# Kernel optimization log

Measured on AMD Instinct MI355X. Metric: run time of the kernel, lower is better.

## Reference

```python
import jax, jax.numpy as jnp
import numpy as np
from jax.ops import segment_sum, segment_max

N_NODES = 100000
N_EDGES = 1600000
F_DIM = 64
N_GRAPHS = 64
K_HOPS = 3
EPS = 1e-5


def setup_inputs() -> dict:
    key = jax.random.key(0)
    ks = jax.random.split(key, 8)
    x = jax.random.normal(ks[0], (N_NODES, F_DIM), dtype=jnp.float32)
    edge_index = jax.random.randint(ks[1], (2, N_EDGES), 0, N_NODES, dtype=jnp.int32)
    batch = jnp.sort(jax.random.randint(ks[2], (N_NODES,), 0, N_GRAPHS, dtype=jnp.int32))
    edge_weight = jax.random.uniform(ks[3], (N_EDGES,), dtype=jnp.float32)
    # TAGConv params: K+1 hop-wise linear weights (no per-lin bias) + one output bias
    W = jax.random.normal(ks[4], (K_HOPS + 1, F_DIM, F_DIM), dtype=jnp.float32) * 0.05
    b = jnp.zeros((F_DIM,), dtype=jnp.float32)
    # GraphNorm params
    gn_weight = jnp.ones((F_DIM,), dtype=jnp.float32)
    gn_bias = jnp.zeros((F_DIM,), dtype=jnp.float32)
    gn_mean_scale = jnp.ones((F_DIM,), dtype=jnp.float32)
    return {"x": x, "edge_index": edge_index, "batch": batch, "edge_weight": edge_weight,
            "W": W, "b": b, "gn_weight": gn_weight, "gn_bias": gn_bias,
            "gn_mean_scale": gn_mean_scale}


def reference(x, edge_index, batch, edge_weight, W, b, gn_weight, gn_bias, gn_mean_scale):
    src, dst = edge_index[0], edge_index[1]

    # --- TAGConv: gcn_norm without self-loops ---
    deg = segment_sum(edge_weight, dst, num_segments=N_NODES)            # [N]
    dis = jnp.where(deg > 0, jax.lax.rsqrt(deg), 0.0)                    # deg^{-1/2}, inf -> 0
    norm = dis[src] * edge_weight * dis[dst]                             # [E]

    # out = sum_k (A_norm^k x) W_k + b
    out = x @ W[0]
    h = x
    for k in range(1, K_HOPS + 1):
        h = segment_sum(norm[:, None] * h[src], dst, num_segments=N_NODES)  # [N, F]
        out = out + h @ W[k]
    out = out + b

    # --- GraphNorm: per-graph mean/var with learnable mean_scale ---
    cnt = segment_sum(jnp.ones((N_NODES,), out.dtype), batch, num_segments=N_GRAPHS)
    cnt = jnp.maximum(cnt, 1.0)[:, None]                                  # [G, 1]
    mean = segment_sum(out, batch, num_segments=N_GRAPHS) / cnt          # [G, F]
    centered = out - mean[batch] * gn_mean_scale                         # [N, F]
    var = segment_sum(centered * centered, batch, num_segments=N_GRAPHS) / cnt
    hn = gn_weight * centered / jnp.sqrt(var + EPS)[batch] + gn_bias

    # --- residual + ReLU (add_residue=True) ---
    h_emb = jax.nn.relu(hn + x)                                          # [N, F]

    # --- global mean + max pooling ---
    mean_pool = segment_sum(h_emb, batch, num_segments=N_GRAPHS) / cnt   # [G, F]
    max_pool = segment_max(h_emb, batch, num_segments=N_GRAPHS)          # [G, F]
    flat = jnp.concatenate([mean_pool, max_pool], axis=-1)               # [G, 2F]

    return (h_emb, flat)
```

## Files before the change

### kernel.cpp

```cpp
#include <hip/hip_runtime.h>
#include <hip/hip_bf16.h>

#define NN 100000
#define NE 1600000
#define NG 64
#define FD 64
#define EPSV 1e-5f

typedef __hip_bfloat16 bf16;
typedef __attribute__((ext_vector_type(8))) short bf16x8;
typedef __attribute__((ext_vector_type(4))) float f32x4;

__device__ __forceinline__ float ldb(bf16 v) { return __bfloat162float(v); }
__device__ __forceinline__ bf16 f2b(float v) { return __float2bfloat16(v); }
__device__ __forceinline__ float b2f_bits(short s) {
    return __uint_as_float(((unsigned)(unsigned short)s) << 16);
}

#define NB1 391
#define CB 625
#define EPB 2560
#define CCN (NB1 * CB)
#define SCB2 ((CCN + 2047) / 2048)

__device__ __forceinline__ int xcd_chunk(int bid, int nwg) {
    int q = nwg >> 3, r = nwg & 7;
    int xcd = bid & 7, j = bid >> 3;
    return (xcd < r ? xcd * (q + 1) : r * (q + 1) + (xcd - r) * q) + j;
}

constexpr size_t ALGN(size_t x) { return (x + 255) & ~(size_t)255; }
constexpr size_t OFF_GSUM = 0;
constexpr size_t OFF_GSSQ = OFF_GSUM + ALGN((size_t)NG * FD * 4);
constexpr size_t OFF_GCNT = OFF_GSSQ + ALGN((size_t)NG * FD * 4);
constexpr size_t OFF_PSUM = OFF_GCNT + ALGN((size_t)NG * 4);
constexpr size_t OFF_PMAX = OFF_PSUM + ALGN((size_t)NG * FD * 4);
constexpr size_t ZERO_BYTES = OFF_PMAX + ALGN((size_t)NG * FD * 4);
constexpr size_t OFF_CNT  = ZERO_BYTES;
constexpr size_t OFF_DIS  = OFF_CNT  + ALGN((size_t)NN * 4);
constexpr size_t OFF_ROWP = OFF_DIS  + ALGN((size_t)NN * 4);
constexpr size_t OFF_BSUM = OFF_ROWP + ALGN((size_t)NN * 4);
constexpr size_t OFF_WT   = OFF_BSUM + ALGN(256 * 4);
constexpr size_t OFF_CSR  = OFF_WT   + ALGN(16384 * 2);
constexpr size_t OFF_H    = OFF_CSR  + ALGN((size_t)NE * 8);
constexpr size_t OFF_OUT  = OFF_H    + ALGN((size_t)NN * 256 * 2);
constexpr size_t OFF_CSRT = OFF_OUT;
constexpr size_t OFF_CC   = OFF_CSRT + ALGN((size_t)NE * 8);
static_assert(OFF_CC + (size_t)CCN * 4 - OFF_OUT <= (size_t)NN * FD * 4, "alias overflow");

#define XCB 25000
__global__ __launch_bounds__(256) void coarse_fused_kernel(const int* __restrict__ dst,
                                                           int* __restrict__ cc,
                                                           const float* __restrict__ x,
                                                           bf16* __restrict__ H,
                                                           const float* __restrict__ W,
                                                           bf16* __restrict__ Wt) {
    int b = blockIdx.x;
    if (b < CB) {
        __shared__ int hist[NB1];
        for (int i = threadIdx.x; i < NB1; i += 256) hist[i] = 0;
        __syncthreads();
        int e0 = b * EPB + threadIdx.x;
        #pragma unroll
        for (int i = 0; i < EPB / 256; i++)
            atomicAdd(&hist[dst[e0 + i * 256] >> 8], 1);
        __syncthreads();
        for (int i = threadIdx.x; i < NB1; i += 256)
            cc[(size_t)i * CB + b] = hist[i];
    } else if (b < CB + XCB) {
        int i = (b - CB) * 256 + threadIdx.x;
        if (i >= NN * 64) return;
        int node = i >> 6, f = i & 63;
        H[(size_t)node * 256 + f] = f2b(x[(size_t)node * 64 + f]);
    } else {
        int i = (b - CB - XCB) * 256 + threadIdx.x;
        int n = i & 63, kk = i >> 6;
        Wt[n * 256 + kk] = f2b(W[kk * 64 + n]);
    }
}

#define SCAN_BLK 256
#define SCAN_ITEMS 8
__global__ __launch_bounds__(SCAN_BLK) void scan_blocks(int* __restrict__ data,
                                                        int* __restrict__ bsum, int n) {
    __shared__ int lds[SCAN_BLK];
    int t = threadIdx.x, b = blockIdx.x;
    int base = b * SCAN_BLK * SCAN_ITEMS + t * SCAN_ITEMS;
    int v[SCAN_ITEMS];
    int s = 0;
    #pragma unroll
    for (int i = 0; i < SCAN_ITEMS; i++) {
        int idx = base + i;
        v[i] = (idx < n) ? data[idx] : 0;
        s += v[i];
    }
    lds[t] = s;
    __syncthreads();
    for (int off = 1; off < SCAN_BLK; off <<= 1) {
        int x = (t >= off) ? lds[t - off] : 0;
        __syncthreads();
        lds[t] += x;
        __syncthreads();
    }
    int excl = lds[t] - s;
    if (t == SCAN_BLK - 1) bsum[b] = lds[t];
    int run = excl;
    #pragma unroll
    for (int i = 0; i < SCAN_ITEMS; i++) {
        int idx = base + i;
        if (idx < n) data[idx] = run;
        run += v[i];
    }
}

__global__ __launch_bounds__(256) void bsum_scan(int* __restrict__ bsum, int nb) {
    __shared__ int lds[256];
    int t = threadIdx.x;
    int v = (t < nb) ? bsum[t] : 0;
    lds[t] = v;
    __syncthreads();
    for (int off = 1; off < 256; off <<= 1) {
        int x = (t >= off) ? lds[t - off] : 0;
        __syncthreads();
        lds[t] += x;
        __syncthreads();
    }
    if (t < nb) bsum[t] = lds[t] - v;
}

__global__ __launch_bounds__(256) void scan_add2(int* __restrict__ data,
                                                 const int* __restrict__ bpref, int n) {
    int i = blockIdx.x * 256 + threadIdx.x;
    if (i >= n) return;
    data[i] += bpref[i >> 11];
}

__global__ __launch_bounds__(256) void scatter2_kernel(const int* __restrict__ src,
                                                       const int* __restrict__ dst,
                                                       const float* __restrict__ ew,
                                                       const int* __restrict__ cc,
                                                       int2* __restrict__ csrt) {
    __shared__ int sc[512];
    __shared__ int gdel[NB1];
    __shared__ int2 stage[EPB];
    __shared__ int sdel[EPB];
    int t = threadIdx.x;
    int L = xcd_chunk(blockIdx.x, CB);

    sc[t] = 0; sc[t + 256] = 0;
    __syncthreads();

    int br[EPB / 256], px[EPB / 256], pw[EPB / 256];
    #pragma unroll
    for (int i = 0; i < EPB / 256; i++) {
        int e = L * EPB + i * 256 + t;
        int d = dst[e];
        int bk = d >> 8;
        int rk = atomicAdd(&sc[bk], 1);
        br[i] = bk | (rk << 9);
        px[i] = src[e] | ((d & 255) << 17);
        pw[i] = __float_as_int(ew[e]);
    }
    __syncthreads();

    for (int off = 1; off < 512; off <<= 1) {
        int a0 = (t >= off) ? sc[t - off] : 0;
        int a1 = sc[t + 256 - off];
        __syncthreads();
        sc[t] += a0; sc[t + 256] += a1;
        __syncthreads();
    }

    for (int i = t; i < NB1; i += 256)
        gdel[i] = cc[(size_t)i * CB + L] - ((i > 0) ? sc[i - 1] : 0);
    __syncthreads();

    #pragma unroll
    for (int i = 0; i < EPB / 256; i++) {
        int bk = br[i] & 511;
        int rk = br[i] >> 9;
        int slot = ((bk > 0) ? sc[bk - 1] : 0) + rk;
        stage[slot] = make_int2(px[i], pw[i]);
        sdel[slot] = gdel[bk];
    }
    __syncthreads();

    for (int j = t; j < EPB; j += 256)
        csrt[(size_t)(sdel[j] + j)] = stage[j];
}

__global__ __launch_bounds__(256) void fine_kernel(const int* __restrict__ cc,
                                                   const int2* __restrict__ csrt,
                                                   int2* __restrict__ csr,
                                                   int* __restrict__ rowp,
                                                   int* __restrict__ cnts,
                                                   float* __restrict__ dis) {
    __shared__ int hist[256];
    __shared__ float degw[256];
    __shared__ int pref[256];
    __shared__ int fcur[256];
    int b = blockIdx.x;
    int t = threadIdx.x;
    int base = cc[(size_t)b * CB];
    int end = (b == NB1 - 1) ? NE : cc[(size_t)(b + 1) * CB];
    int cnt = end - base;
    hist[t] = 0; degw[t] = 0.f;
    __syncthreads();
    for (int j = t; j < cnt; j += 256) {
        int2 e = csrt[base + j];
        int f = e.x >> 17;
        atomicAdd(&hist[f], 1);
        atomicAdd(&degw[f], __int_as_float(e.y));
    }
    __syncthreads();
    int hv = hist[t];
    pref[t] = hv;
    __syncthreads();
    for (int off = 1; off < 256; off <<= 1) {
        int x = (t >= off) ? pref[t - off] : 0;
        __syncthreads();
        pref[t] += x;
        __syncthreads();
    }
    int ex = pref[t] - hv;
    fcur[t] = ex;
    int node = b * 256 + t;
    if (node < NN) {
        rowp[node] = base + ex;
        cnts[node] = hv;
        float s = degw[t];
        dis[node] = (s > 0.f) ? rsqrtf(s) : 0.f;
    }
    __syncthreads();
    for (int j = t; j < cnt; j += 256) {
        int2 e = csrt[base + j];
        int f = e.x >> 17;
        int pos = atomicAdd(&fcur[f], 1);
        csr[base + pos] = make_int2(e.x & 0x1FFFF, e.y);
    }
}

template <bool FIRST>
__global__ __launch_bounds__(256) void hop_kernel(const bf16* __restrict__ hin,
                                                  bf16* __restrict__ hout,
                                                  const int* __restrict__ rowp,
                                                  const int* __restrict__ cnts,
                                                  int2* __restrict__ csr,
                                                  const float* __restrict__ dis) {
    int row = blockIdx.x * 4 + (threadIdx.x >> 6);
    if (row >= NN) return;
    row = __builtin_amdgcn_readfirstlane(row);
    int lane = threadIdx.x & 63;
    int sub = lane >> 3;
    int fl = lane & 7;
    int start = rowp[row];
    int cnt = cnts[row];
    float dr = dis[row];
    int2* cp = csr + start;

    float a[8] = {0, 0, 0, 0, 0, 0, 0, 0};

    if (cnt <= 24) {
        int2 e0 = (sub < cnt) ? cp[sub] : make_int2(0, 0);
        int2 e1 = (8 + sub < cnt) ? cp[8 + sub] : make_int2(0, 0);
        int2 e2 = (16 + sub < cnt) ? cp[16 + sub] : make_int2(0, 0);
        bf16x8 v0 = *(const bf16x8*)(hin + (size_t)e0.x * 256 + fl * 8);
        bf16x8 v1 = *(const bf16x8*)(hin + (size_t)e1.x * 256 + fl * 8);
        bf16x8 v2 = *(const bf16x8*)(hin + (size_t)e2.x * 256 + fl * 8);
        float w0 = __int_as_float(e0.y);
        float w1 = __int_as_float(e1.y);
        float w2 = __int_as_float(e2.y);
        if (FIRST) {
            w0 *= dis[e0.x]; w1 *= dis[e1.x]; w2 *= dis[e2.x];
            if (fl == 0) {
                if (sub < cnt)      cp[sub].y      = __float_as_int(w0);
                if (8 + sub < cnt)  cp[8 + sub].y  = __float_as_int(w1);
                if (16 + sub < cnt) cp[16 + sub].y = __float_as_int(w2);
            }
        }
        #pragma unroll
        for (int i = 0; i < 8; i++)
            a[i] = w0 * b2f_bits(v0[i]) + w1 * b2f_bits(v1[i]) + w2 * b2f_bits(v2[i]);
    } else {
        float b[8] = {0, 0, 0, 0, 0, 0, 0, 0};
        int j = 0;
        for (; j + 16 <= cnt; j += 16) {
            int2 e0 = cp[j + sub];
            int2 e1 = cp[j + 8 + sub];
            bf16x8 v0 = *(const bf16x8*)(hin + (size_t)e0.x * 256 + fl * 8);
            bf16x8 v1 = *(const bf16x8*)(hin + (size_t)e1.x * 256 + fl * 8);
            float w0 = __int_as_float(e0.y);
            float w1 = __int_as_float(e1.y);
            if (FIRST) {
                w0 *= dis[e0.x]; w1 *= dis[e1.x];
                if (fl == 0) {
                    cp[j + sub].y     = __float_as_int(w0);
                    cp[j + 8 + sub].y = __float_as_int(w1);
                }
            }
            #pragma unroll
            for (int i = 0; i < 8; i++) a[i] += w0 * b2f_bits(v0[i]);
            #pragma unroll
            for (int i = 0; i < 8; i++) b[i] += w1 * b2f_bits(v1[i]);
        }
        for (; j < cnt; j += 8) {
            int jj = j + sub;
            int2 e = (jj < cnt) ? cp[jj] : make_int2(0, 0);
            bf16x8 v = *(const bf16x8*)(hin + (size_t)e.x * 256 + fl * 8);
            float w = __int_as_float(e.y);
            if (FIRST) {
                w *= dis[e.x];
                if (fl == 0 && jj < cnt) cp[jj].y = __float_as_int(w);
            }
            #pragma unroll
            for (int i = 0; i < 8; i++) a[i] += w * b2f_bits(v[i]);
        }
        #pragma unroll
        for (int i = 0; i < 8; i++) a[i] += b[i];
    }

    #pragma unroll
    for (int i = 0; i < 8; i++) a[i] += __shfl_xor(a[i], 8);
    #pragma unroll
    for (int i = 0; i < 8; i++) a[i] += __shfl_xor(a[i], 16);
    #pragma unroll
    for (int i = 0; i < 8; i++) a[i] += __shfl_xor(a[i], 32);

    if (sub == 0) {
        bf16x8 ov;
        #pragma unroll
        for (int i = 0; i < 8; i++) {
            bf16 t = f2b(a[i] * dr);
            ov[i] = *(short*)&t;
        }
        *(bf16x8*)(hout + (size_t)row * 256 + fl * 8) = ov;
    }
}

__global__ __launch_bounds__(256) void gemm_kernel(const bf16* __restrict__ H,
                                                   const bf16* __restrict__ Wt,
                                                   const float* __restrict__ bias,
                                                   float* __restrict__ outb) {
    int row0 = blockIdx.x * 16;
    int wave = threadIdx.x >> 6;
    int lane = threadIdx.x & 63;
    int m = lane & 15, q = lane >> 4;
    int c0 = wave * 16;

    bf16x8 A[8];
    const bf16* arow = H + (size_t)(row0 + m) * 256 + q * 8;
    #pragma unroll
    for (int ks = 0; ks < 8; ks++)
        A[ks] = *(const bf16x8*)(arow + ks * 32);

    const bf16* brow = Wt + (size_t)(c0 + m) * 256 + q * 8;
    f32x4 acc = {0.f, 0.f, 0.f, 0.f};
    #pragma unroll
    for (int ks = 0; ks < 8; ks++) {
        bf16x8 B = *(const bf16x8*)(brow + ks * 32);
        acc = __builtin_amdgcn_mfma_f32_16x16x32_bf16(A[ks], B, acc, 0, 0, 0);
    }

    float bv = bias[c0 + m];
    #pragma unroll
    for (int r = 0; r < 4; r++)
        outb[(size_t)(row0 + q * 4 + r) * 64 + c0 + m] = acc[r] + bv;
}

#define CH 32
#define STAT_WAVES ((NN + CH - 1) / CH)
#define STAT_BLOCKS ((STAT_WAVES * 64 + 255) / 256)

__global__ __launch_bounds__(256) void stats_kernel(const float* __restrict__ outb,
                                                    const int* __restrict__ batch,
                                                    float* __restrict__ gsum,
                                                    float* __restrict__ gssq,
                                                    float* __restrict__ gcnt) {
    int wid = (blockIdx.x * 256 + threadIdx.x) >> 6;
    int lane = threadIdx.x & 63;
    int n0 = wid * CH;
    if (n0 >= NN) return;
    int n1 = min(n0 + CH, NN);
    int g0 = batch[n0];
    if (n1 == n0 + CH && batch[n1 - 1] == g0) {
        float s = 0.f, s2 = 0.f;
        #pragma unroll
        for (int i = 0; i < CH; i++) {
            float v = outb[(size_t)(n0 + i) * 64 + lane];
            s += v; s2 += v * v;
        }
        atomicAdd(&gsum[g0 * 64 + lane], s);
        atomicAdd(&gssq[g0 * 64 + lane], s2);
        if (lane == 0) atomicAdd(&gcnt[g0], (float)CH);
    } else {
        int cur = g0; float s = 0.f, s2 = 0.f; int cl = 0;
        for (int i = n0; i < n1; i++) {
            int g = batch[i];
            if (g != cur) {
                atomicAdd(&gsum[cur * 64 + lane], s);
                atomicAdd(&gssq[cur * 64 + lane], s2);
                if (lane == 0) atomicAdd(&gcnt[cur], (float)cl);
                s = 0.f; s2 = 0.f; cl = 0; cur = g;
            }
            float v = outb[(size_t)i * 64 + lane];
            s += v; s2 += v * v; cl++;
        }
        atomicAdd(&gsum[cur * 64 + lane], s);
        atomicAdd(&gssq[cur * 64 + lane], s2);
        if (lane == 0) atomicAdd(&gcnt[cur], (float)cl);
    }
}

__device__ __forceinline__ void graph_mr(const float* gsum, const float* gssq,
                                         const float* gcnt, int g, int lane, float ms,
                                         float& mm, float& r) {
    float c = fmaxf(gcnt[g], 1.f);
    float mean = gsum[g * 64 + lane] / c;
    float msq = gssq[g * 64 + lane] / c;
    mm = mean * ms;
    float var = fmaxf(msq - 2.f * mm * mean + mm * mm, 0.f);
    r = rsqrtf(var + EPSV);
}

__global__ __launch_bounds__(256) void final_kernel(const float* __restrict__ outb,
                                                    const int* __restrict__ batch,
                                                    const float* __restrict__ xg,
                                                    const float* __restrict__ gsum,
                                                    const float* __restrict__ gssq,
                                                    const float* __restrict__ gcnt,
                                                    const float* __restrict__ gw_,
                                                    const float* __restrict__ gb_,
                                                    const float* __restrict__ ms_,
                                                    float* __restrict__ psum,
                                                    int* __restrict__ pmax,
                                                    float* __restrict__ hemb) {
    int wid = (blockIdx.x * 256 + threadIdx.x) >> 6;
    int lane = threadIdx.x & 63;
    int n0 = wid * CH;
    if (n0 >= NN) return;
    int n1 = min(n0 + CH, NN);
    float gw = gw_[lane], gb = gb_[lane], ms = ms_[lane];
    int g0 = batch[n0];
    if (n1 == n0 + CH && batch[n1 - 1] == g0) {
        float m, r;
        graph_mr(gsum, gssq, gcnt, g0, lane, ms, m, r);
        float ps = 0.f, pm = 0.f;
        #pragma unroll
        for (int i = 0; i < CH; i++) {
            size_t idx = (size_t)(n0 + i) * 64 + lane;
            float hn = gw * (outb[idx] - m) * r + gb;
            float he = hn + xg[idx];
            he = he > 0.f ? he : 0.f;
            hemb[idx] = he;
            ps += he;
            pm = fmaxf(pm, he);
        }
        atomicAdd(&psum[g0 * 64 + lane], ps);
        atomicMax(&pmax[g0 * 64 + lane], __float_as_int(pm));
    } else {
        int cur = g0;
        float m, r;
        graph_mr(gsum, gssq, gcnt, cur, lane, ms, m, r);
        float ps = 0.f, pm = 0.f;
        for (int i = n0; i < n1; i++) {
            int g = batch[i];
            if (g != cur) {
                atomicAdd(&psum[cur * 64 + lane], ps);
                atomicMax(&pmax[cur * 64 + lane], __float_as_int(pm));
                ps = 0.f; pm = 0.f; cur = g;
                graph_mr(gsum, gssq, gcnt, cur, lane, ms, m, r);
            }
            size_t idx = (size_t)i * 64 + lane;
            float hn = gw * (outb[idx] - m) * r + gb;
            float he = hn + xg[idx];
            he = he > 0.f ? he : 0.f;
            hemb[idx] = he;
            ps += he;
            pm = fmaxf(pm, he);
        }
        atomicAdd(&psum[cur * 64 + lane], ps);
        atomicMax(&pmax[cur * 64 + lane], __float_as_int(pm));
    }
}

__global__ __launch_bounds__(256) void pool_kernel(const float* __restrict__ psum,
                                                   const int* __restrict__ pmax,
                                                   const float* __restrict__ gcnt,
                                                   float* __restrict__ flat) {
    int i = blockIdx.x * 256 + threadIdx.x;
    if (i >= NG * FD) return;
    int g = i >> 6, f = i & 63;
    float c = fmaxf(gcnt[g], 1.f);
    flat[(size_t)g * 128 + f] = psum[i] / c;
    flat[(size_t)g * 128 + 64 + f] = __int_as_float(pmax[i]);
}

extern "C" void kernel_launch(void* const* d_in, const int* in_sizes, int n_in,
                              void* d_out, int out_size, void* d_ws, size_t ws_size,
                              hipStream_t stream) {
    const float* x = (const float*)d_in[0];
    const int* ei = (const int*)d_in[1];
    const int* batch = (const int*)d_in[2];
    const float* ew = (const float*)d_in[3];
    const float* W = (const float*)d_in[4];
    const float* bias = (const float*)d_in[5];
    const float* gnw = (const float*)d_in[6];
    const float* gnb = (const float*)d_in[7];
    const float* gms = (const float*)d_in[8];

    const int* src = ei;
    const int* dst = ei + NE;

    char* ws = (char*)d_ws;
    float* gsum = (float*)(ws + OFF_GSUM);
    float* gssq = (float*)(ws + OFF_GSSQ);
    float* gcnt = (float*)(ws + OFF_GCNT);
    float* psum = (float*)(ws + OFF_PSUM);
    int* pmax = (int*)(ws + OFF_PMAX);
    int* cnts = (int*)(ws + OFF_CNT);
    float* dis = (float*)(ws + OFF_DIS);
    int* rowp = (int*)(ws + OFF_ROWP);
    int* bsum = (int*)(ws + OFF_BSUM);
    bf16* Wt = (bf16*)(ws + OFF_WT);
    int2* csr = (int2*)(ws + OFF_CSR);
    bf16* H = (bf16*)(ws + OFF_H);
    float* outb = (float*)(ws + OFF_OUT);
    int2* csrt = (int2*)(ws + OFF_CSRT);
    int* cc = (int*)(ws + OFF_CC);

    float* hemb = (float*)d_out;
    float* flat = hemb + (size_t)NN * FD;

    hipMemsetAsync(d_ws, 0, ZERO_BYTES, stream);

    const int HOPB = (NN + 3) / 4;
    const int GFB = (NG * FD + 255) / 256;
    const int ADDB = (CCN + 255) / 256;

    coarse_fused_kernel<<<CB + XCB + 64, 256, 0, stream>>>(dst, cc, x, H, W, Wt);
    scan_blocks<<<SCB2, 256, 0, stream>>>(cc, bsum, CCN);
    bsum_scan<<<1, 256, 0, stream>>>(bsum, SCB2);
    scan_add2<<<ADDB, 256, 0, stream>>>(cc, bsum, CCN);
    scatter2_kernel<<<CB, 256, 0, stream>>>(src, dst, ew, cc, csrt);
    fine_kernel<<<NB1, 256, 0, stream>>>(cc, csrt, csr, rowp, cnts, dis);

    hop_kernel<true><<<HOPB, 256, 0, stream>>>(H, H + 64, rowp, cnts, csr, dis);
    hop_kernel<false><<<HOPB, 256, 0, stream>>>(H + 64, H + 128, rowp, cnts, csr, dis);
    hop_kernel<false><<<HOPB, 256, 0, stream>>>(H + 128, H + 192, rowp, cnts, csr, dis);

    gemm_kernel<<<NN / 16, 256, 0, stream>>>(H, Wt, bias, outb);

    stats_kernel<<<STAT_BLOCKS, 256, 0, stream>>>(outb, batch, gsum, gssq, gcnt);
    final_kernel<<<STAT_BLOCKS, 256, 0, stream>>>(outb, batch, x, gsum, gssq, gcnt,
                                                  gnw, gnb, gms, psum, pmax, hemb);
    pool_kernel<<<GFB, 256, 0, stream>>>(psum, pmax, gcnt, flat);
}
```

Baseline: 382.6 us.

## Make GEMM persistent with register-resident weights and double-buffered A tiles

The final GEMM now runs as a persistent grid of 1024 waves. Each wave loads all of Wt (64x256 bf16) and the bias into registers once, then loops over 16-row tiles with a grid stride. Loads of the next A tile are double-buffered so they overlap the MFMAs of the current one. This removes the redundant per-block weight loads and per-tile launch overhead, at the cost of very high register pressure (launch_bounds 256,1) and lower occupancy.

```diff
diff --git a/kernel.cpp b/kernel.cpp
--- a/kernel.cpp
+++ b/kernel.cpp
@@ -337,34 +337,72 @@
     }
 }
 
-__global__ __launch_bounds__(256) void gemm_kernel(const bf16* __restrict__ H,
-                                                   const bf16* __restrict__ Wt,
-                                                   const float* __restrict__ bias,
-                                                   float* __restrict__ outb) {
-    int row0 = blockIdx.x * 16;
+#define GWAVES 1024
+#define NT (NN / 16)
+
+__global__ __launch_bounds__(256, 1) void gemm_kernel(const bf16* __restrict__ H,
+                                                      const bf16* __restrict__ Wt,
+                                                      const float* __restrict__ bias,
+                                                      float* __restrict__ outb) {
     int wave = threadIdx.x >> 6;
     int lane = threadIdx.x & 63;
     int m = lane & 15, q = lane >> 4;
-    int c0 = wave * 16;
-
-    bf16x8 A[8];
-    const bf16* arow = H + (size_t)(row0 + m) * 256 + q * 8;
-    #pragma unroll
-    for (int ks = 0; ks < 8; ks++)
-        A[ks] = *(const bf16x8*)(arow + ks * 32);
-
-    const bf16* brow = Wt + (size_t)(c0 + m) * 256 + q * 8;
-    f32x4 acc = {0.f, 0.f, 0.f, 0.f};
-    #pragma unroll
-    for (int ks = 0; ks < 8; ks++) {
-        bf16x8 B = *(const bf16x8*)(brow + ks * 32);
-        acc = __builtin_amdgcn_mfma_f32_16x16x32_bf16(A[ks], B, acc, 0, 0, 0);
-    }
-
-    float bv = bias[c0 + m];
-    #pragma unroll
-    for (int r = 0; r < 4; r++)
-        outb[(size_t)(row0 + q * 4 + r) * 64 + c0 + m] = acc[r] + bv;
+    int w = blockIdx.x * 4 + wave;
+
+    bf16x8 B[4][8];
+    #pragma unroll
+    for (int n = 0; n < 4; n++) {
+        const bf16* brow = Wt + (size_t)(n * 16 + m) * 256 + q * 8;
+        #pragma unroll
+        for (int ks = 0; ks < 8; ks++) B[n][ks] = *(const bf16x8*)(brow + ks * 32);
+    }
+    float bv[4];
+    #pragma unroll
+    for (int n = 0; n < 4; n++) bv[n] = bias[n * 16 + m];
+
+    if (w >= NT) return;
+
+    bf16x8 A0[8], A1[8];
+
+    #define LOADA(dst_, t_)                                                  \
+        {                                                                    \
+            const bf16* arow = H + (size_t)((t_)*16 + m) * 256 + q * 8;      \
+            _Pragma("unroll")                                                \
+            for (int ks = 0; ks < 8; ks++)                                   \
+                dst_[ks] = *(const bf16x8*)(arow + ks * 32);                 \
+        }
+
+    #define COMP(src_, t_)                                                   \
+        {                                                                    \
+            _Pragma("unroll")                                                \
+            for (int n = 0; n < 4; n++) {                                    \
+                f32x4 acc = {0.f, 0.f, 0.f, 0.f};                            \
+                _Pragma("unroll")                                            \
+                for (int ks = 0; ks < 8; ks++)                               \
+                    acc = __builtin_amdgcn_mfma_f32_16x16x32_bf16(           \
+                        src_[ks], B[n][ks], acc, 0, 0, 0);                   \
+                _Pragma("unroll")                                            \
+                for (int r = 0; r < 4; r++)                                  \
+                    outb[(size_t)((t_)*16 + q * 4 + r) * 64 + n * 16 + m] =  \
+                        acc[r] + bv[n];                                      \
+            }                                                                \
+        }
+
+    int t = w;
+    LOADA(A0, t)
+    while (true) {
+        int t1 = t + GWAVES;
+        if (t1 < NT) LOADA(A1, t1)
+        COMP(A0, t)
+        if (t1 >= NT) return;
+        int t2 = t1 + GWAVES;
+        if (t2 < NT) LOADA(A0, t2)
+        COMP(A1, t1)
+        if (t2 >= NT) return;
+        t = t2;
+    }
+    #undef LOADA
+    #undef COMP
 }
 
 #define CH 32
@@ -548,7 +586,7 @@
     hop_kernel<false><<<HOPB, 256, 0, stream>>>(H + 64, H + 128, rowp, cnts, csr, dis);
     hop_kernel<false><<<HOPB, 256, 0, stream>>>(H + 128, H + 192, rowp, cnts, csr, dis);
 
-    gemm_kernel<<<NN / 16, 256, 0, stream>>>(H, Wt, bias, outb);
+    gemm_kernel<<<GWAVES / 4, 256, 0, stream>>>(H, Wt, bias, outb);
 
     stats_kernel<<<STAT_BLOCKS, 256, 0, stream>>>(outb, batch, gsum, gssq, gcnt);
     final_kernel<<<STAT_BLOCKS, 256, 0, stream>>>(outb, batch, x, gsum, gssq, gcnt,
```

Measured after the change: 353.5 us. -7.6%, faster.
